# Kernel optimization log

Measured on AMD Instinct MI355X. Metric: run time of the kernel, lower is better.

## Reference

```python
import jax, jax.numpy as jnp
import numpy as np

N_QUBITS = 12
K_STEPS = 6
VOCAB = 32000
D_EMB = 512
N_CLASSES = 8
B = 256
SEQ = 128
DIM = 2 ** N_QUBITS


def apply_1q(psi, U, q):
    # psi: [B, 2^n]; U: [2,2] (shared) or [B,2,2] (per-sample). Apply on wire q
    # (PennyLane convention: wire 0 = most significant axis).
    b = psi.shape[0]
    left, right = 2 ** q, 2 ** (N_QUBITS - q - 1)
    st = psi.reshape(b, left, 2, right)
    if U.ndim == 3:
        st = jnp.einsum('bij,bajr->bair', U, st)
    else:
        st = jnp.einsum('ij,bajr->bair', U, st)
    return st.reshape(b, DIM)


def apply_cnot(psi, c, t):
    b = psi.shape[0]
    st = psi.reshape((b,) + (2,) * N_QUBITS)
    c_ax, t_ax = 1 + c, 1 + t
    c0 = jnp.take(st, 0, axis=c_ax)
    c1 = jnp.take(st, 1, axis=c_ax)
    t_ax2 = t_ax - 1 if t_ax > c_ax else t_ax  # axis shift after take
    c1 = jnp.flip(c1, axis=t_ax2)
    return jnp.stack([c0, c1], axis=c_ax).reshape(b, DIM)


def ry_mat(angle):
    # angle: [B] -> [B,2,2] complex64
    c = jnp.cos(angle / 2)
    s = jnp.sin(angle / 2)
    row0 = jnp.stack([c, -s], axis=-1)
    row1 = jnp.stack([s, c], axis=-1)
    return jnp.stack([row0, row1], axis=-2).astype(jnp.complex64)


def rot_mat(phi, theta, omega):
    # PennyLane Rot(phi, theta, omega) = RZ(omega) RY(theta) RZ(phi)
    c = jnp.cos(theta / 2)
    s = jnp.sin(theta / 2)
    ep = jnp.exp(-0.5j * (phi + omega).astype(jnp.complex64))
    em = jnp.exp(0.5j * (phi - omega).astype(jnp.complex64))
    m = jnp.stack([jnp.stack([ep * c, -em * s]), jnp.stack([jnp.conj(em) * s, jnp.conj(ep) * c])])
    return m.astype(jnp.complex64)


def block(psi, x, theta_k):
    # data reupload RY(x_i), trainable Rot, ring of CNOTs (noiseless)
    for i in range(N_QUBITS):
        psi = apply_1q(psi, ry_mat(x[:, i]), i)
    for i in range(N_QUBITS):
        psi = apply_1q(psi, rot_mat(theta_k[i, 0], theta_k[i, 1], theta_k[i, 2]), i)
    for i in range(N_QUBITS - 1):
        psi = apply_cnot(psi, i, i + 1)
    psi = apply_cnot(psi, N_QUBITS - 1, 0)
    return psi


def z_expvals(psi):
    # <Z_i> for all wires from |psi|^2
    b = psi.shape[0]
    p = (psi.real ** 2 + psi.imag ** 2).reshape((b,) + (2,) * N_QUBITS)
    zs = []
    for i in range(N_QUBITS):
        axes = tuple(ax for ax in range(1, N_QUBITS + 1) if ax != 1 + i)
        m = p.sum(axis=axes)  # [B,2]
        zs.append(m[:, 0] - m[:, 1])
    return jnp.stack(zs, axis=-1)  # [B, n_qubits]


def _forward(input_ids, attention_mask, emb_table, proj_w, proj_b, theta, head_w, head_b):
    # encoder: embed -> masked mean pool -> tanh(linear) * pi
    e = emb_table[input_ids]                              # [B,S,D]
    mask = attention_mask[:, :, None].astype(jnp.float32)
    pooled = (e * mask).sum(axis=1) / jnp.clip(mask.sum(axis=1), 1.0)
    x = jnp.tanh(pooled @ proj_w.T + proj_b) * jnp.float32(np.pi)  # [B, n_qubits]

    b = x.shape[0]
    psi = jnp.zeros((b, DIM), jnp.complex64).at[:, 0].set(1.0)
    readouts = []
    for k in range(K_STEPS):
        psi = block(psi, x, theta[k])
        readouts.append(z_expvals(psi))
    step_readouts = jnp.stack(readouts, axis=0)           # [K,B,n_qubits]
    step_logits = step_readouts @ head_w.T + head_b       # [K,B,n_classes]
    return step_logits, step_readouts, step_logits[-1]


def setup_inputs() -> dict:
    key = jax.random.key(0)
    ks = jax.random.split(key, 6)
    input_ids = jax.random.randint(ks[0], (B, SEQ), 0, VOCAB)
    attention_mask = jnp.ones((B, SEQ), dtype=jnp.int32)
    emb_table = jax.random.normal(ks[1], (VOCAB, D_EMB), jnp.float32)
    emb_table = emb_table.at[0].set(0.0)  # padding_idx=0 row is zeros
    proj_w = jax.random.normal(ks[2], (N_QUBITS, D_EMB), jnp.float32) / np.sqrt(D_EMB)
    proj_b = jnp.zeros((N_QUBITS,), jnp.float32)
    theta = 0.01 * jax.random.normal(ks[3], (K_STEPS, N_QUBITS, 3), jnp.float32)
    head_w = jax.random.normal(ks[4], (N_CLASSES, N_QUBITS), jnp.float32) / np.sqrt(N_QUBITS)
    head_b = jnp.zeros((N_CLASSES,), jnp.float32)
    return {'input_ids': input_ids, 'attention_mask': attention_mask,
            'emb_table': emb_table, 'proj_w': proj_w, 'proj_b': proj_b,
            'theta': theta, 'head_w': head_w, 'head_b': head_b}


def reference(input_ids, attention_mask, emb_table, proj_w, proj_b, theta, head_w, head_b):
    return _forward(input_ids, attention_mask, emb_table, proj_w, proj_b, theta, head_w, head_b)
```

## Files before the change

### kernel.cpp

```cpp
#include <hip/hip_runtime.h>
#include <math.h>

#define NQ 12
#define DIM 4096
#define KS 6
#define BB 256
#define SEQ 128
#define DEMB 512


#define REG_GATE(P, W) { \
    float4 c0 = *(const float4*)&s_u[k][W][0]; \
    float4 c1 = *(const float4*)&s_u[k][W][4]; \
    float u00r=c0.x,u00i=c0.y,u01r=c0.z,u01i=c0.w; \
    float u10r=c1.x,u10i=c1.y,u11r=c1.z,u11i=c1.w; \
    _Pragma("unroll") \
    for (int r0 = 0; r0 < 8; ++r0) if (!(r0 & (1 << (P)))) { \
        int r1 = r0 | (1 << (P)); \
        float2 A = a[r0], Bv = a[r1]; \
        a[r0].x = u00r*A.x - u00i*A.y + u01r*Bv.x - u01i*Bv.y; \
        a[r0].y = u00r*A.y + u00i*A.x + u01r*Bv.y + u01i*Bv.x; \
        a[r1].x = u10r*A.x - u10i*A.y + u11r*Bv.x - u11i*Bv.y; \
        a[r1].y = u10r*A.y + u10i*A.x + u11r*Bv.y + u11i*Bv.x; \
    } }

#define SHUF_GATE(MK, W) { \
    float4 c0 = *(const float4*)&s_u[k][W][0]; \
    float4 c1 = *(const float4*)&s_u[k][W][4]; \
    int bit_ = (lane & (MK)) != 0; \
    float c0r = bit_ ? c1.z : c0.x; \
    float c0i = bit_ ? c1.w : c0.y; \
    float c1r = bit_ ? c1.x : c0.z; \
    float c1i = bit_ ? c1.y : c0.w; \
    _Pragma("unroll") \
    for (int r = 0; r < 8; ++r) { \
        float px = __shfl_xor(a[r].x, MK, 64); \
        float py = __shfl_xor(a[r].y, MK, 64); \
        float nx = c0r*a[r].x - c0i*a[r].y + c1r*px - c1i*py; \
        float ny = c0r*a[r].y + c0i*a[r].x + c1r*py + c1i*px; \
        a[r].x = nx; a[r].y = ny; \
    } }

#define PL(v, m) v += __shfl_xor(v, m, 64);

__device__ __forceinline__ int swz14(int x) { return x ^ ((x >> 4) & 14); }

__global__ __launch_bounds__(512) void fused_kernel(
    const int* __restrict__ ids, const int* __restrict__ mask,
    const float* __restrict__ emb, const float* __restrict__ pw,
    const float* __restrict__ pb, const float* __restrict__ theta,
    const float* __restrict__ hw, const float* __restrict__ hb,
    float* __restrict__ readouts, float* __restrict__ logits,
    float* __restrict__ last)
{
    __shared__ __align__(16) float2 buf0[DIM];
    __shared__ __align__(16) float2 buf1[DIM];
    __shared__ __align__(16) float  s_u[KS][NQ][8];
    __shared__ float  s_red[8][NQ];
    __shared__ float  s_msum[4];
    __shared__ float  s_wred[2][NQ];
    __shared__ float  s_x[NQ];
    __shared__ float  s_hw[8 * NQ];
    __shared__ float  s_hb[8];

    int b = blockIdx.x;
    int tid = threadIdx.x;
    int lane = tid & 63, wave = tid >> 6;

    int*   s_ids = (int*)buf1;
    float* s_m   = (float*)buf1 + SEQ;
    float4* s_part = (float4*)buf0;

    if (tid < SEQ) {
        s_ids[tid] = ids[b * SEQ + tid];
        s_m[tid]   = (float)mask[b * SEQ + tid];
    }
    if (tid >= 256 && tid < 256 + 8 * NQ) s_hw[tid - 256] = hw[tid - 256];
    if (tid >= 384 && tid < 392)          s_hb[tid - 384] = hb[tid - 384];
    __syncthreads();

    {
        int g = tid >> 7, e = tid & 127;
        float4 acc = make_float4(0.f, 0.f, 0.f, 0.f);
        float msum = 0.f;
        #pragma unroll 8
        for (int s = g; s < SEQ; s += 4) {
            float m = s_m[s];
            float4 v = ((const float4*)emb)[(size_t)s_ids[s] * 128 + e];
            acc.x = fmaf(m, v.x, acc.x);
            acc.y = fmaf(m, v.y, acc.y);
            acc.z = fmaf(m, v.z, acc.z);
            acc.w = fmaf(m, v.w, acc.w);
            msum += m;
        }
        __syncthreads();
        s_part[g * 128 + e] = acc;
        if (e == 0) s_msum[g] = msum;
    }
    __syncthreads();

    if (tid < 128) {
        float tm = fmaxf(s_msum[0] + s_msum[1] + s_msum[2] + s_msum[3], 1.f);
        float inv = 1.f / tm;
        float4 p0 = s_part[0 * 128 + tid], p1 = s_part[1 * 128 + tid];
        float4 p2 = s_part[2 * 128 + tid], p3 = s_part[3 * 128 + tid];
        float4 p;
        p.x = (p0.x + p1.x + p2.x + p3.x) * inv;
        p.y = (p0.y + p1.y + p2.y + p3.y) * inv;
        p.z = (p0.z + p1.z + p2.z + p3.z) * inv;
        p.w = (p0.w + p1.w + p2.w + p3.w) * inv;
        float z[NQ];
        #pragma unroll
        for (int i = 0; i < NQ; ++i) {
            float4 w4 = ((const float4*)pw)[i * 128 + tid];
            z[i] = p.x * w4.x + p.y * w4.y + p.z * w4.z + p.w * w4.w;
        }
        #pragma unroll
        for (int i = 0; i < NQ; ++i) {
            #pragma unroll
            for (int off = 32; off > 0; off >>= 1)
                z[i] += __shfl_xor(z[i], off, 64);
        }
        if ((tid & 63) == 0) {
            int w = tid >> 6;
            #pragma unroll
            for (int i = 0; i < NQ; ++i) s_wred[w][i] = z[i];
        }
    }
    __syncthreads();
    if (tid < NQ) {
        float d = pb[tid] + s_wred[0][tid] + s_wred[1][tid];
        s_x[tid] = tanhf(d) * 3.14159274101257324f;
    }
    __syncthreads();

    if (tid < KS * NQ) {
        int k = tid / NQ, w = tid % NQ;
        float ang = s_x[w];
        float cy = cosf(0.5f * ang), sy = sinf(0.5f * ang);
        const float* th = theta + (k * NQ + w) * 3;
        float phi = th[0], te = th[1], om = th[2];
        float ct = cosf(0.5f * te), st = sinf(0.5f * te);
        float a1 = -0.5f * (phi + om);
        float epr = cosf(a1), epi = sinf(a1);
        float a2 = 0.5f * (phi - om);
        float emr = cosf(a2), emi = sinf(a2);
        float R00r = epr * ct,  R00i = epi * ct;
        float R01r = -emr * st, R01i = -emi * st;
        float R10r = emr * st,  R10i = -emi * st;
        float R11r = epr * ct,  R11i = -epi * ct;
        s_u[k][w][0] =  R00r * cy + R01r * sy;
        s_u[k][w][1] =  R00i * cy + R01i * sy;
        s_u[k][w][2] = -R00r * sy + R01r * cy;
        s_u[k][w][3] = -R00i * sy + R01i * cy;
        s_u[k][w][4] =  R10r * cy + R11r * sy;
        s_u[k][w][5] =  R10i * cy + R11i * sy;
        s_u[k][w][6] = -R10r * sy + R11r * cy;
        s_u[k][w][7] = -R10i * sy + R11i * cy;
    }

    int T8 = tid << 3;
    int baseA  = swz14(T8);
    int baseA4 = baseA >> 1;
    int addrE[8], idxP[8];
    #pragma unroll
    for (int r = 0; r < 8; ++r) {
        int jE = wave | (lane << 3) | (r << 9);
        addrE[r] = swz14(jE);
        int b0 = (jE >> 11) & 1;
        int pref = b0, outv = 0;
        for (int w = 1; w < NQ; ++w) {
            pref ^= (jE >> (11 - w)) & 1;
            outv |= pref << (11 - w);
        }
        outv |= (b0 ^ pref) << 11;
        idxP[r] = swz14(outv);
    }

    float2 a[8];
    #pragma unroll
    for (int r = 0; r < 8; ++r) a[r] = make_float2(0.f, 0.f);
    if (tid == 0) a[0].x = 1.f;
    __syncthreads();

    for (int k = 0; k < KS; ++k) {
        if (k > 0) {
            float p[8];
            #pragma unroll
            for (int r = 0; r < 8; ++r)
                p[r] = a[r].x * a[r].x + a[r].y * a[r].y;
            float e0=p[0]+p[1], d0=p[0]-p[1], e1=p[2]+p[3], d1=p[2]-p[3];
            float e2=p[4]+p[5], d2=p[4]-p[5], e3=p[6]+p[7], d3=p[6]-p[7];
            float T   = e0+e1+e2+e3;
            float S11 = d0+d1+d2+d3;
            float S10 = (e0-e1)+(e2-e3);
            float S9  = (e0+e1)-(e2+e3);
            float c = T, x;
            x = __shfl_xor(c,1,64);  float V8=(lane&1)? x-c:c-x;  c+=x;
            PL(V8,2) PL(V8,4) PL(V8,8) PL(V8,16) PL(V8,32)
            x = __shfl_xor(c,2,64);  float V7=(lane&2)? x-c:c-x;  c+=x;
            PL(V7,4) PL(V7,8) PL(V7,16) PL(V7,32)
            x = __shfl_xor(c,4,64);  float V6=(lane&4)? x-c:c-x;  c+=x;
            PL(V6,8) PL(V6,16) PL(V6,32)
            x = __shfl_xor(c,8,64);  float V5=(lane&8)? x-c:c-x;  c+=x;
            PL(V5,16) PL(V5,32)
            x = __shfl_xor(c,16,64); float V4=(lane&16)? x-c:c-x; c+=x;
            PL(V4,32)
            x = __shfl_xor(c,32,64); float V3=(lane&32)? x-c:c-x; c+=x;
            PL(S11,1) PL(S11,2) PL(S11,4) PL(S11,8) PL(S11,16) PL(S11,32)
            PL(S10,1) PL(S10,2) PL(S10,4) PL(S10,8) PL(S10,16) PL(S10,32)
            PL(S9,1)  PL(S9,2)  PL(S9,4)  PL(S9,8)  PL(S9,16)  PL(S9,32)
            if (lane == 0) {
                float* sr = s_red[wave];
                sr[11] = S11; sr[10] = S10; sr[9] = S9;
                sr[8] = V8; sr[7] = V7; sr[6] = V6;
                sr[5] = V5; sr[4] = V4; sr[3] = V3;
                sr[2] = (wave & 1) ? -c : c;
                sr[1] = (wave & 2) ? -c : c;
                sr[0] = (wave & 4) ? -c : c;
            }
        }

        REG_GATE(0, 11) REG_GATE(1, 10) REG_GATE(2, 9)
        SHUF_GATE(1, 8) SHUF_GATE(2, 7) SHUF_GATE(4, 6)

        #pragma unroll
        for (int i = 0; i < 4; ++i)
            ((float4*)buf0)[baseA4 ^ i] =
                make_float4(a[2*i].x, a[2*i].y, a[2*i+1].x, a[2*i+1].y);
        __syncthreads();

        if (k > 0) {
            if (tid < NQ) {
                float s = 0.f;
                #pragma unroll
                for (int w2 = 0; w2 < 8; ++w2) s += s_red[w2][tid];
                readouts[((k-1) * BB + b) * NQ + tid] = s;
            }
            if (tid < 8) {
                float acc2 = s_hb[tid];
                #pragma unroll
                for (int i = 0; i < NQ; ++i) {
                    float si = 0.f;
                    #pragma unroll
                    for (int w2 = 0; w2 < 8; ++w2) si += s_red[w2][i];
                    acc2 = fmaf(si, s_hw[tid * NQ + i], acc2);
                }
                logits[((k-1) * BB + b) * 8 + tid] = acc2;
            }
        }

        #pragma unroll
        for (int r = 0; r < 8; ++r) a[r] = buf0[addrE[r]];

        REG_GATE(0, 2) REG_GATE(1, 1) REG_GATE(2, 0)
        SHUF_GATE(8, 5) SHUF_GATE(16, 4) SHUF_GATE(32, 3)

        #pragma unroll
        for (int r = 0; r < 8; ++r) buf1[idxP[r]] = a[r];
        __syncthreads();
        #pragma unroll
        for (int i = 0; i < 4; ++i) {
            float4 v = ((float4*)buf1)[baseA4 ^ i];
            a[2*i]   = make_float2(v.x, v.y);
            a[2*i+1] = make_float2(v.z, v.w);
        }
    }

    {
        float p[8];
        #pragma unroll
        for (int r = 0; r < 8; ++r)
            p[r] = a[r].x * a[r].x + a[r].y * a[r].y;
        float e0=p[0]+p[1], d0=p[0]-p[1], e1=p[2]+p[3], d1=p[2]-p[3];
        float e2=p[4]+p[5], d2=p[4]-p[5], e3=p[6]+p[7], d3=p[6]-p[7];
        float T   = e0+e1+e2+e3;
        float S11 = d0+d1+d2+d3;
        float S10 = (e0-e1)+(e2-e3);
        float S9  = (e0+e1)-(e2+e3);
        float c = T, x;
        x = __shfl_xor(c,1,64);  float V8=(lane&1)? x-c:c-x;  c+=x;
        PL(V8,2) PL(V8,4) PL(V8,8) PL(V8,16) PL(V8,32)
        x = __shfl_xor(c,2,64);  float V7=(lane&2)? x-c:c-x;  c+=x;
        PL(V7,4) PL(V7,8) PL(V7,16) PL(V7,32)
        x = __shfl_xor(c,4,64);  float V6=(lane&4)? x-c:c-x;  c+=x;
        PL(V6,8) PL(V6,16) PL(V6,32)
        x = __shfl_xor(c,8,64);  float V5=(lane&8)? x-c:c-x;  c+=x;
        PL(V5,16) PL(V5,32)
        x = __shfl_xor(c,16,64); float V4=(lane&16)? x-c:c-x; c+=x;
        PL(V4,32)
        x = __shfl_xor(c,32,64); float V3=(lane&32)? x-c:c-x; c+=x;
        PL(S11,1) PL(S11,2) PL(S11,4) PL(S11,8) PL(S11,16) PL(S11,32)
        PL(S10,1) PL(S10,2) PL(S10,4) PL(S10,8) PL(S10,16) PL(S10,32)
        PL(S9,1)  PL(S9,2)  PL(S9,4)  PL(S9,8)  PL(S9,16)  PL(S9,32)
        if (lane == 0) {
            float* sr = s_red[wave];
            sr[11] = S11; sr[10] = S10; sr[9] = S9;
            sr[8] = V8; sr[7] = V7; sr[6] = V6;
            sr[5] = V5; sr[4] = V4; sr[3] = V3;
            sr[2] = (wave & 1) ? -c : c;
            sr[1] = (wave & 2) ? -c : c;
            sr[0] = (wave & 4) ? -c : c;
        }
    }
    __syncthreads();
    if (tid < NQ) {
        float s = 0.f;
        #pragma unroll
        for (int w2 = 0; w2 < 8; ++w2) s += s_red[w2][tid];
        readouts[((KS-1) * BB + b) * NQ + tid] = s;
    }
    if (tid < 8) {
        float acc2 = s_hb[tid];
        #pragma unroll
        for (int i = 0; i < NQ; ++i) {
            float si = 0.f;
            #pragma unroll
            for (int w2 = 0; w2 < 8; ++w2) si += s_red[w2][i];
            acc2 = fmaf(si, s_hw[tid * NQ + i], acc2);
        }
        logits[((KS-1) * BB + b) * 8 + tid] = acc2;
        last[b * 8 + tid] = acc2;
    }
}

extern "C" void kernel_launch(void* const* d_in, const int* in_sizes, int n_in,
                              void* d_out, int out_size, void* d_ws, size_t ws_size,
                              hipStream_t stream) {
    const int*   ids   = (const int*)d_in[0];
    const int*   mask  = (const int*)d_in[1];
    const float* emb   = (const float*)d_in[2];
    const float* pw    = (const float*)d_in[3];
    const float* pb    = (const float*)d_in[4];
    const float* theta = (const float*)d_in[5];
    const float* hw    = (const float*)d_in[6];
    const float* hb    = (const float*)d_in[7];
    float* out = (float*)d_out;

    float* readouts = out + KS * BB * 8;
    float* last     = out + KS * BB * 8 + KS * BB * NQ;

    fused_kernel<<<BB, 512, 0, stream>>>(ids, mask, emb, pw, pb, theta,
                                         hw, hb, readouts, out, last);
}
```

Before: 144.7 us.

## Use DPP lane swaps for gates and reductions, remap lanes, split gather accumulators

```diff
diff --git a/kernel.cpp b/kernel.cpp
--- a/kernel.cpp
+++ b/kernel.cpp
@@ -8,6 +8,9 @@
 #define SEQ 128
 #define DEMB 512
 
+
+#define DPP_XOR1(v) __int_as_float(__builtin_amdgcn_mov_dpp(__float_as_int(v), 0xB1, 0xF, 0xF, true))
+#define DPP_XOR2(v) __int_as_float(__builtin_amdgcn_mov_dpp(__float_as_int(v), 0x4E, 0xF, 0xF, true))
 
 #define REG_GATE(P, W) { \
     float4 c0 = *(const float4*)&s_u[k][W][0]; \
@@ -41,9 +44,67 @@
         a[r].x = nx; a[r].y = ny; \
     } }
 
+#define DPP_GATE(MK, W, DPPF) { \
+    float4 c0 = *(const float4*)&s_u[k][W][0]; \
+    float4 c1 = *(const float4*)&s_u[k][W][4]; \
+    int bit_ = (lane & (MK)) != 0; \
+    float c0r = bit_ ? c1.z : c0.x; \
+    float c0i = bit_ ? c1.w : c0.y; \
+    float c1r = bit_ ? c1.x : c0.z; \
+    float c1i = bit_ ? c1.y : c0.w; \
+    _Pragma("unroll") \
+    for (int r = 0; r < 8; ++r) { \
+        float px = DPPF(a[r].x); \
+        float py = DPPF(a[r].y); \
+        float nx = c0r*a[r].x - c0i*a[r].y + c1r*px - c1i*py; \
+        float ny = c0r*a[r].y + c0i*a[r].x + c1r*py + c1i*px; \
+        a[r].x = nx; a[r].y = ny; \
+    } }
+
 #define PL(v, m) v += __shfl_xor(v, m, 64);
 
 __device__ __forceinline__ int swz14(int x) { return x ^ ((x >> 4) & 14); }
+
+__device__ __forceinline__ void expval_LA(const float2* a, int lane, int wave,
+                                          float sr[][NQ]) {
+    float p[8];
+    #pragma unroll
+    for (int r = 0; r < 8; ++r)
+        p[r] = a[r].x * a[r].x + a[r].y * a[r].y;
+    float e0=p[0]+p[1], d0=p[0]-p[1], e1=p[2]+p[3], d1=p[2]-p[3];
+    float e2=p[4]+p[5], d2=p[4]-p[5], e3=p[6]+p[7], d3=p[6]-p[7];
+    float T   = e0+e1+e2+e3;
+    float S11 = d0+d1+d2+d3;
+    float S10 = (e0-e1)+(e2-e3);
+    float S9  = (e0+e1)-(e2+e3);
+    float c = T, x;
+    x = DPP_XOR1(c);        float V8=(lane&1)? x-c:c-x;  c+=x;
+    V8 += DPP_XOR2(V8); PL(V8,4) PL(V8,8) PL(V8,16) PL(V8,32)
+    x = DPP_XOR2(c);        float V7=(lane&2)? x-c:c-x;  c+=x;
+    PL(V7,4) PL(V7,8) PL(V7,16) PL(V7,32)
+    x = __shfl_xor(c,4,64);  float V6=(lane&4)? x-c:c-x;  c+=x;
+    PL(V6,8) PL(V6,16) PL(V6,32)
+    x = __shfl_xor(c,8,64);  float V5=(lane&8)? x-c:c-x;  c+=x;
+    PL(V5,16) PL(V5,32)
+    x = __shfl_xor(c,16,64); float V4=(lane&16)? x-c:c-x; c+=x;
+    PL(V4,32)
+    x = __shfl_xor(c,32,64); float V3=(lane&32)? x-c:c-x; c+=x;
+    S11 += DPP_XOR1(S11); S11 += DPP_XOR2(S11);
+    PL(S11,4) PL(S11,8) PL(S11,16) PL(S11,32)
+    S10 += DPP_XOR1(S10); S10 += DPP_XOR2(S10);
+    PL(S10,4) PL(S10,8) PL(S10,16) PL(S10,32)
+    S9  += DPP_XOR1(S9);  S9  += DPP_XOR2(S9);
+    PL(S9,4)  PL(S9,8)  PL(S9,16)  PL(S9,32)
+    if (lane == 0) {
+        float* o = sr[wave];
+        o[11] = S11; o[10] = S10; o[9] = S9;
+        o[8] = V8; o[7] = V7; o[6] = V6;
+        o[5] = V5; o[4] = V4; o[3] = V3;
+        o[2] = (wave & 1) ? -c : c;
+        o[1] = (wave & 2) ? -c : c;
+        o[0] = (wave & 4) ? -c : c;
+    }
+}
 
 __global__ __launch_bounds__(512) void fused_kernel(
     const int* __restrict__ ids, const int* __restrict__ mask,
@@ -81,20 +142,26 @@
 
     {
         int g = tid >> 7, e = tid & 127;
-        float4 acc = make_float4(0.f, 0.f, 0.f, 0.f);
+        float4 acc0 = make_float4(0.f, 0.f, 0.f, 0.f);
+        float4 acc1 = make_float4(0.f, 0.f, 0.f, 0.f);
         float msum = 0.f;
+        const float4* emb4 = (const float4*)emb;
         #pragma unroll 8
-        for (int s = g; s < SEQ; s += 4) {
-            float m = s_m[s];
-            float4 v = ((const float4*)emb)[(size_t)s_ids[s] * 128 + e];
-            acc.x = fmaf(m, v.x, acc.x);
-            acc.y = fmaf(m, v.y, acc.y);
-            acc.z = fmaf(m, v.z, acc.z);
-            acc.w = fmaf(m, v.w, acc.w);
-            msum += m;
-        }
+        for (int t = 0; t < 32; t += 2) {
+            int sA = g + 4 * t, sB = sA + 4;
+            float mA = s_m[sA], mB = s_m[sB];
+            float4 vA = emb4[(size_t)s_ids[sA] * 128 + e];
+            float4 vB = emb4[(size_t)s_ids[sB] * 128 + e];
+            acc0.x = fmaf(mA, vA.x, acc0.x); acc0.y = fmaf(mA, vA.y, acc0.y);
+            acc0.z = fmaf(mA, vA.z, acc0.z); acc0.w = fmaf(mA, vA.w, acc0.w);
+            acc1.x = fmaf(mB, vB.x, acc1.x); acc1.y = fmaf(mB, vB.y, acc1.y);
+            acc1.z = fmaf(mB, vB.z, acc1.z); acc1.w = fmaf(mB, vB.w, acc1.w);
+            msum += mA + mB;
+        }
+        acc0.x += acc1.x; acc0.y += acc1.y;
+        acc0.z += acc1.z; acc0.w += acc1.w;
         __syncthreads();
-        s_part[g * 128 + e] = acc;
+        s_part[g * 128 + e] = acc0;
         if (e == 0) s_msum[g] = msum;
     }
     __syncthreads();
@@ -165,7 +232,7 @@
     int addrE[8], idxP[8];
     #pragma unroll
     for (int r = 0; r < 8; ++r) {
-        int jE = wave | (lane << 3) | (r << 9);
+        int jE = wave | (((lane >> 3) & 7) << 3) | ((lane & 7) << 6) | (r << 9);
         addrE[r] = swz14(jE);
         int b0 = (jE >> 11) & 1;
         int pref = b0, outv = 0;
@@ -184,45 +251,12 @@
     __syncthreads();
 
     for (int k = 0; k < KS; ++k) {
-        if (k > 0) {
-            float p[8];
-            #pragma unroll
-            for (int r = 0; r < 8; ++r)
-                p[r] = a[r].x * a[r].x + a[r].y * a[r].y;
-            float e0=p[0]+p[1], d0=p[0]-p[1], e1=p[2]+p[3], d1=p[2]-p[3];
-            float e2=p[4]+p[5], d2=p[4]-p[5], e3=p[6]+p[7], d3=p[6]-p[7];
-            float T   = e0+e1+e2+e3;
-            float S11 = d0+d1+d2+d3;
-            float S10 = (e0-e1)+(e2-e3);
-            float S9  = (e0+e1)-(e2+e3);
-            float c = T, x;
-            x = __shfl_xor(c,1,64);  float V8=(lane&1)? x-c:c-x;  c+=x;
-            PL(V8,2) PL(V8,4) PL(V8,8) PL(V8,16) PL(V8,32)
-            x = __shfl_xor(c,2,64);  float V7=(lane&2)? x-c:c-x;  c+=x;
-            PL(V7,4) PL(V7,8) PL(V7,16) PL(V7,32)
-            x = __shfl_xor(c,4,64);  float V6=(lane&4)? x-c:c-x;  c+=x;
-            PL(V6,8) PL(V6,16) PL(V6,32)
-            x = __shfl_xor(c,8,64);  float V5=(lane&8)? x-c:c-x;  c+=x;
-            PL(V5,16) PL(V5,32)
-            x = __shfl_xor(c,16,64); float V4=(lane&16)? x-c:c-x; c+=x;
-            PL(V4,32)
-            x = __shfl_xor(c,32,64); float V3=(lane&32)? x-c:c-x; c+=x;
-            PL(S11,1) PL(S11,2) PL(S11,4) PL(S11,8) PL(S11,16) PL(S11,32)
-            PL(S10,1) PL(S10,2) PL(S10,4) PL(S10,8) PL(S10,16) PL(S10,32)
-            PL(S9,1)  PL(S9,2)  PL(S9,4)  PL(S9,8)  PL(S9,16)  PL(S9,32)
-            if (lane == 0) {
-                float* sr = s_red[wave];
-                sr[11] = S11; sr[10] = S10; sr[9] = S9;
-                sr[8] = V8; sr[7] = V7; sr[6] = V6;
-                sr[5] = V5; sr[4] = V4; sr[3] = V3;
-                sr[2] = (wave & 1) ? -c : c;
-                sr[1] = (wave & 2) ? -c : c;
-                sr[0] = (wave & 4) ? -c : c;
-            }
-        }
+        if (k > 0) expval_LA(a, lane, wave, s_red);
 
         REG_GATE(0, 11) REG_GATE(1, 10) REG_GATE(2, 9)
-        SHUF_GATE(1, 8) SHUF_GATE(2, 7) SHUF_GATE(4, 6)
+        DPP_GATE(1, 8, DPP_XOR1)
+        DPP_GATE(2, 7, DPP_XOR2)
+        SHUF_GATE(4, 6)
 
         #pragma unroll
         for (int i = 0; i < 4; ++i)
@@ -254,7 +288,9 @@
         for (int r = 0; r < 8; ++r) a[r] = buf0[addrE[r]];
 
         REG_GATE(0, 2) REG_GATE(1, 1) REG_GATE(2, 0)
-        SHUF_GATE(8, 5) SHUF_GATE(16, 4) SHUF_GATE(32, 3)
+        DPP_GATE(1, 5, DPP_XOR1)
+        DPP_GATE(2, 4, DPP_XOR2)
+        SHUF_GATE(4, 3)
 
         #pragma unroll
         for (int r = 0; r < 8; ++r) buf1[idxP[r]] = a[r];
@@ -267,42 +303,7 @@
         }
     }
 
-    {
-        float p[8];
-        #pragma unroll
-        for (int r = 0; r < 8; ++r)
-            p[r] = a[r].x * a[r].x + a[r].y * a[r].y;
-        float e0=p[0]+p[1], d0=p[0]-p[1], e1=p[2]+p[3], d1=p[2]-p[3];
-        float e2=p[4]+p[5], d2=p[4]-p[5], e3=p[6]+p[7], d3=p[6]-p[7];
-        float T   = e0+e1+e2+e3;
-        float S11 = d0+d1+d2+d3;
-        float S10 = (e0-e1)+(e2-e3);
-        float S9  = (e0+e1)-(e2+e3);
-        float c = T, x;
-        x = __shfl_xor(c,1,64);  float V8=(lane&1)? x-c:c-x;  c+=x;
-        PL(V8,2) PL(V8,4) PL(V8,8) PL(V8,16) PL(V8,32)
-        x = __shfl_xor(c,2,64);  float V7=(lane&2)? x-c:c-x;  c+=x;
-        PL(V7,4) PL(V7,8) PL(V7,16) PL(V7,32)
-        x = __shfl_xor(c,4,64);  float V6=(lane&4)? x-c:c-x;  c+=x;
-        PL(V6,8) PL(V6,16) PL(V6,32)
-        x = __shfl_xor(c,8,64);  float V5=(lane&8)? x-c:c-x;  c+=x;
-        PL(V5,16) PL(V5,32)
-        x = __shfl_xor(c,16,64); float V4=(lane&16)? x-c:c-x; c+=x;
-        PL(V4,32)
-        x = __shfl_xor(c,32,64); float V3=(lane&32)? x-c:c-x; c+=x;
-        PL(S11,1) PL(S11,2) PL(S11,4) PL(S11,8) PL(S11,16) PL(S11,32)
-        PL(S10,1) PL(S10,2) PL(S10,4) PL(S10,8) PL(S10,16) PL(S10,32)
-        PL(S9,1)  PL(S9,2)  PL(S9,4)  PL(S9,8)  PL(S9,16)  PL(S9,32)
-        if (lane == 0) {
-            float* sr = s_red[wave];
-            sr[11] = S11; sr[10] = S10; sr[9] = S9;
-            sr[8] = V8; sr[7] = V7; sr[6] = V6;
-            sr[5] = V5; sr[4] = V4; sr[3] = V3;
-            sr[2] = (wave & 1) ? -c : c;
-            sr[1] = (wave & 2) ? -c : c;
-            sr[0] = (wave & 4) ? -c : c;
-        }
-    }
+    expval_LA(a, lane, wave, s_red);
     __syncthreads();
     if (tid < NQ) {
         float s = 0.f;
```

Measured after the change: 141.5 us. 1.02x faster.
